# Optimization experiments

Measured on AMD Instinct MI355X. Metric: run time of the kernel, lower is better.

Reference implementation:

```python
import jax, jax.numpy as jnp
import numpy as np

B, T, I, H, O = 256, 2048, 64, 64, 2


def setup_inputs() -> dict:
    key = jax.random.key(0)
    ks = jax.random.split(key, 12)
    s = lambda fan_in: 1.0 / np.sqrt(fan_in)
    u = lambda k, shape, b: jax.random.uniform(k, shape, jnp.float32, -b, b)
    return {
        "x": jax.random.normal(ks[0], (B, T, I), jnp.float32),
        # RNN layer 0 (input -> hidden)
        "W_ih0": u(ks[1], (H, I), s(H)),
        "W_hh0": u(ks[2], (H, H), s(H)),
        "b_ih0": u(ks[3], (H,), s(H)),
        "b_hh0": u(ks[4], (H,), s(H)),
        # RNN layer 1 (hidden -> hidden)
        "W_ih1": u(ks[5], (H, H), s(H)),
        "W_hh1": u(ks[6], (H, H), s(H)),
        "b_ih1": u(ks[7], (H,), s(H)),
        "b_hh1": u(ks[8], (H,), s(H)),
        # MLP head
        "W1": u(ks[9], (H, H), s(H)),
        "b1": u(ks[10], (H,), s(H)),
        "W2": u(ks[11], (O, H), s(H)),
        "b2": jnp.zeros((O,), jnp.float32),
    }


def _rnn_layer(x, W_ih, W_hh, b_ih, b_hh):
    # x: (B, T, D_in) -> (B, T, H); h_t = tanh(x_t W_ih^T + b_ih + h_{t-1} W_hh^T + b_hh)
    # Precompute the input projection for all timesteps (one big GEMM).
    xin = jnp.einsum("btd,hd->bth", x, W_ih) + b_ih + b_hh  # (B,T,H)

    def step(h, xt):
        h_new = jnp.tanh(xt + h @ W_hh.T)
        return h_new, h_new

    h0 = jnp.zeros((x.shape[0], W_hh.shape[0]), x.dtype)
    _, hs = jax.lax.scan(step, h0, jnp.swapaxes(xin, 0, 1))  # (T,B,H)
    return jnp.swapaxes(hs, 0, 1)  # (B,T,H)


def reference(x, W_ih0, W_hh0, b_ih0, b_hh0, W_ih1, W_hh1, b_ih1, b_hh1, W1, b1, W2, b2):
    h = _rnn_layer(x, W_ih0, W_hh0, b_ih0, b_hh0)
    h = _rnn_layer(h, W_ih1, W_hh1, b_ih1, b_hh1)
    # MLP head (dropout disabled in inference): Linear -> ReLU -> Linear
    z = jax.nn.relu(jnp.einsum("bth,oh->bto", h, W1) + b1)
    out = jnp.einsum("bth,oh->bto", z, W2) + b2
    return out
```

## Files before the change

kernel.cpp:

```cpp
#include <hip/hip_runtime.h>


#define T_LEN 2048
#define K     16
#define NITV  (T_LEN / K)

__device__ __forceinline__ float tanh_fast(float x) {
  float e = __expf(2.0f * x);
  return 1.0f - 2.0f / (e + 1.0f);
}

__device__ __forceinline__ float dot64(const float* v, const float (&w)[64]) {
  float a0 = 0.f, a1 = 0.f, a2 = 0.f, a3 = 0.f;
#pragma unroll
  for (int k = 0; k < 64; k += 4) {
    float4 h = *(const float4*)(v + k);
    a0 = fmaf(h.x, w[k + 0], a0);
    a1 = fmaf(h.y, w[k + 1], a1);
    a2 = fmaf(h.z, w[k + 2], a2);
    a3 = fmaf(h.w, w[k + 3], a3);
  }
  return (a0 + a1) + (a2 + a3);
}

__device__ __forceinline__ float dot32(const float* v, const float (&w)[32]) {
  float a0 = 0.f, a1 = 0.f, a2 = 0.f, a3 = 0.f;
#pragma unroll
  for (int k = 0; k < 32; k += 4) {
    float4 h = *(const float4*)(v + k);
    a0 = fmaf(h.x, w[k + 0], a0);
    a1 = fmaf(h.y, w[k + 1], a1);
    a2 = fmaf(h.z, w[k + 2], a2);
    a3 = fmaf(h.w, w[k + 3], a3);
  }
  return (a0 + a1) + (a2 + a3);
}

__global__ __launch_bounds__(256, 1) void rnn_fused(
    const float* __restrict__ x,
    const float* __restrict__ Wih0, const float* __restrict__ Whh0,
    const float* __restrict__ bih0, const float* __restrict__ bhh0,
    const float* __restrict__ Wih1, const float* __restrict__ Whh1,
    const float* __restrict__ bih1, const float* __restrict__ bhh1,
    const float* __restrict__ W1, const float* __restrict__ b1,
    const float* __restrict__ W2, const float* __restrict__ b2,
    float* __restrict__ out) {
  __shared__ __align__(16) float Xc [2][K][64];
  __shared__ __align__(16) float A0b[2][K][64];
  __shared__ __align__(16) float H0b[2][K][64];
  __shared__ __align__(16) float A1b[2][K][64];
  __shared__ __align__(16) float H1b[2][K][64];
  __shared__ __align__(16) float Zb [2][K][64];
  __shared__ __align__(16) float OutL[T_LEN * 2];

  const int tid  = threadIdx.x;
  const int wave = tid >> 6;
  const int lane = tid & 63;
  const int b    = blockIdx.x;

  if (tid < 64)        H0b[1][K - 1][lane] = 0.f;
  else if (tid < 128)  H1b[1][K - 1][lane] = 0.f;

  {
    const float* src = x + (size_t)b * T_LEN * 64;
    *(float4*)(&Xc[0][0][0] + tid * 4) = *(const float4*)(src + tid * 4);
  }

  const float* wsrc = (wave == 0) ? Wih0 : (wave == 1) ? Whh0 : (wave == 2) ? Wih1 : Whh1;
  float w[64];
#pragma unroll
  for (int q = 0; q < 16; ++q) {
    float4 v = *(const float4*)(wsrc + lane * 64 + 4 * q);
    w[4 * q + 0] = v.x; w[4 * q + 1] = v.y; w[4 * q + 2] = v.z; w[4 * q + 3] = v.w;
  }
  float bias = 0.f;
  if (wave == 0) bias = bih0[lane] + bhh0[lane];
  else if (wave == 2) bias = bih1[lane] + bhh1[lane];

  const int kh = (lane >> 5) * 32;
  const int jz = (lane & 31) + ((wave == 2) ? 32 : 0);
  float wE[32];
  float bE = 0.f;
  if (wave == 0 || wave == 2) {
#pragma unroll
    for (int q = 0; q < 8; ++q) {
      float4 v = *(const float4*)(W1 + jz * 64 + kh + 4 * q);
      wE[4 * q + 0] = v.x; wE[4 * q + 1] = v.y; wE[4 * q + 2] = v.z; wE[4 * q + 3] = v.w;
    }
    bE = b1[jz];
  }

  const int tj = lane >> 2, kq = lane & 3;
  float wF0[16], wF1[16];
  float b20 = 0.f, b21 = 0.f;
  if (wave == 2) {
#pragma unroll
    for (int q = 0; q < 4; ++q) {
      float4 v0 = *(const float4*)(W2 + kq * 16 + 4 * q);
      float4 v1 = *(const float4*)(W2 + 64 + kq * 16 + 4 * q);
      wF0[4 * q + 0] = v0.x; wF0[4 * q + 1] = v0.y; wF0[4 * q + 2] = v0.z; wF0[4 * q + 3] = v0.w;
      wF1[4 * q + 0] = v1.x; wF1[4 * q + 1] = v1.y; wF1[4 * q + 2] = v1.z; wF1[4 * q + 3] = v1.w;
    }
    b20 = b2[0]; b21 = b2[1];
  }

  __syncthreads();

  for (int n = 0; n < NITV + 5; ++n) {
    if (wave == 0) {
      float4 px[4];
      const bool pf = (n + 1) < NITV;
      if (pf) {
        const float* src = x + ((size_t)b * T_LEN + (size_t)(n + 1) * K) * 64 + lane * 4;
#pragma unroll
        for (int r = 0; r < 4; ++r) px[r] = *(const float4*)(src + r * 256);
      }
      if (n < NITV) {
        const int s = n & 1;
#pragma unroll
        for (int j = 0; j < K; ++j) {
          A0b[s][j][lane] = bias + dot64(&Xc[s][j][0], w);
        }
      }
      if (n >= 4 && n - 4 < NITV) {
        const int s = (n - 4) & 1;
#pragma unroll
        for (int j = 0; j < K; ++j) {
          float p = dot32(&H1b[s][j][kh], wE);
          p += __shfl_xor(p, 32);
          if (lane < 32) Zb[s][j][jz] = fmaxf(p + bE, 0.f);
        }
      }
      if (pf) {
        float* dst = &Xc[(n + 1) & 1][0][0] + lane * 4;
#pragma unroll
        for (int r = 0; r < 4; ++r) *(float4*)(dst + r * 256) = px[r];
      }
    } else if (wave == 1) {
      if (n >= 1 && n - 1 < NITV) {
        const int s = (n - 1) & 1;
        float av[K];
#pragma unroll
        for (int j = 0; j < K; ++j) av[j] = A0b[s][j][lane];
        const float* prev = &H0b[s ^ 1][K - 1][0];
#pragma unroll
        for (int j = 0; j < K; ++j) {
          float r = dot64(prev, w);
          H0b[s][j][lane] = tanh_fast(av[j] + r);
          prev = &H0b[s][j][0];
        }
      }
    } else if (wave == 2) {
      if (n >= 2 && n - 2 < NITV) {
        const int s = (n - 2) & 1;
#pragma unroll
        for (int j = 0; j < K; ++j) {
          A1b[s][j][lane] = bias + dot64(&H0b[s][j][0], w);
        }
      }
      if (n >= 4 && n - 4 < NITV) {
        const int s = (n - 4) & 1;
#pragma unroll
        for (int j = 0; j < K; ++j) {
          float p = dot32(&H1b[s][j][kh], wE);
          p += __shfl_xor(p, 32);
          if (lane < 32) Zb[s][j][jz] = fmaxf(p + bE, 0.f);
        }
      }
      if (n >= 5 && n - 5 < NITV) {
        const int s = (n - 5) & 1;
        float p0 = 0.f, p1 = 0.f;
#pragma unroll
        for (int q = 0; q < 4; ++q) {
          float4 zv = *(const float4*)(&Zb[s][tj][kq * 16 + 4 * q]);
          p0 = fmaf(zv.x, wF0[4 * q + 0], p0); p1 = fmaf(zv.x, wF1[4 * q + 0], p1);
          p0 = fmaf(zv.y, wF0[4 * q + 1], p0); p1 = fmaf(zv.y, wF1[4 * q + 1], p1);
          p0 = fmaf(zv.z, wF0[4 * q + 2], p0); p1 = fmaf(zv.z, wF1[4 * q + 2], p1);
          p0 = fmaf(zv.w, wF0[4 * q + 3], p0); p1 = fmaf(zv.w, wF1[4 * q + 3], p1);
        }
        p0 += __shfl_xor(p0, 1); p0 += __shfl_xor(p0, 2);
        p1 += __shfl_xor(p1, 1); p1 += __shfl_xor(p1, 2);
        if (kq == 0) {
          const int t = (n - 5) * K + tj;
          OutL[t * 2 + 0] = p0 + b20;
          OutL[t * 2 + 1] = p1 + b21;
        }
      }
    } else {
      if (n >= 3 && n - 3 < NITV) {
        const int s = (n - 3) & 1;
        float av[K];
#pragma unroll
        for (int j = 0; j < K; ++j) av[j] = A1b[s][j][lane];
        const float* prev = &H1b[s ^ 1][K - 1][0];
#pragma unroll
        for (int j = 0; j < K; ++j) {
          float r = dot64(prev, w);
          H1b[s][j][lane] = tanh_fast(av[j] + r);
          prev = &H1b[s][j][0];
        }
      }
    }
    __syncthreads();
  }

  float* obase = out + (size_t)b * T_LEN * 2;
#pragma unroll
  for (int r = 0; r < 4; ++r) {
    const int fi = r * 256 + tid;
    *(float4*)(obase + fi * 4) = *(const float4*)(OutL + fi * 4);
  }
}

extern "C" void kernel_launch(void* const* d_in, const int* in_sizes, int n_in,
                              void* d_out, int out_size, void* d_ws, size_t ws_size,
                              hipStream_t stream) {
  (void)in_sizes; (void)n_in; (void)d_ws; (void)ws_size; (void)out_size;
  const float* x    = (const float*)d_in[0];
  const float* Wih0 = (const float*)d_in[1];
  const float* Whh0 = (const float*)d_in[2];
  const float* bih0 = (const float*)d_in[3];
  const float* bhh0 = (const float*)d_in[4];
  const float* Wih1 = (const float*)d_in[5];
  const float* Whh1 = (const float*)d_in[6];
  const float* bih1 = (const float*)d_in[7];
  const float* bhh1 = (const float*)d_in[8];
  const float* W1   = (const float*)d_in[9];
  const float* b1   = (const float*)d_in[10];
  const float* W2   = (const float*)d_in[11];
  const float* b2   = (const float*)d_in[12];
  float* out = (float*)d_out;

  rnn_fused<<<dim3(256), dim3(256), 0, stream>>>(
      x, Wih0, Whh0, bih0, bhh0, Wih1, Whh1, bih1, bhh1, W1, b1, W2, b2, out);
}
```

Baseline: 1.253 ms.

## Restructure RNN pipeline with readlane recurrence, 64-step chunks, and swizzled LDS

The recurrent waves now keep the hidden state in registers and broadcast it with readlane instead of re-reading it from LDS every step. The chunk size grows from 16 to 64 timesteps, which cuts the number of block-wide barriers. The input-projection and MLP waves switch to a one-timestep-per-lane layout with uniform weight loads, and a swizzled LDS layout avoids bank conflicts. Output is written directly to global memory. The risks are the 64 serial readlanes per step on the critical recurrence path and longer pipeline fill and drain.

```diff
diff --git a/kernel.cpp b/kernel.cpp
--- a/kernel.cpp
+++ b/kernel.cpp
@@ -2,38 +2,12 @@
 
 
 #define T_LEN 2048
-#define K     16
-#define NITV  (T_LEN / K)
-
-__device__ __forceinline__ float tanh_fast(float x) {
-  float e = __expf(2.0f * x);
-  return 1.0f - 2.0f / (e + 1.0f);
-}
-
-__device__ __forceinline__ float dot64(const float* v, const float (&w)[64]) {
-  float a0 = 0.f, a1 = 0.f, a2 = 0.f, a3 = 0.f;
-#pragma unroll
-  for (int k = 0; k < 64; k += 4) {
-    float4 h = *(const float4*)(v + k);
-    a0 = fmaf(h.x, w[k + 0], a0);
-    a1 = fmaf(h.y, w[k + 1], a1);
-    a2 = fmaf(h.z, w[k + 2], a2);
-    a3 = fmaf(h.w, w[k + 3], a3);
-  }
-  return (a0 + a1) + (a2 + a3);
-}
-
-__device__ __forceinline__ float dot32(const float* v, const float (&w)[32]) {
-  float a0 = 0.f, a1 = 0.f, a2 = 0.f, a3 = 0.f;
-#pragma unroll
-  for (int k = 0; k < 32; k += 4) {
-    float4 h = *(const float4*)(v + k);
-    a0 = fmaf(h.x, w[k + 0], a0);
-    a1 = fmaf(h.y, w[k + 1], a1);
-    a2 = fmaf(h.z, w[k + 2], a2);
-    a3 = fmaf(h.w, w[k + 3], a3);
-  }
-  return (a0 + a1) + (a2 + a3);
+#define BATCH 64
+#define NITV  (T_LEN / BATCH)
+#define NLOOP (NITV + 5)
+
+__device__ __forceinline__ int swz(int t, int c) {
+  return t * 64 + ((((c >> 2) ^ (t & 7)) << 2) | (c & 3));
 }
 
 __global__ __launch_bounds__(256, 1) void rnn_fused(
@@ -45,170 +19,189 @@
     const float* __restrict__ W1, const float* __restrict__ b1,
     const float* __restrict__ W2, const float* __restrict__ b2,
     float* __restrict__ out) {
-  __shared__ __align__(16) float Xc [2][K][64];
-  __shared__ __align__(16) float A0b[2][K][64];
-  __shared__ __align__(16) float H0b[2][K][64];
-  __shared__ __align__(16) float A1b[2][K][64];
-  __shared__ __align__(16) float H1b[2][K][64];
-  __shared__ __align__(16) float Zb [2][K][64];
-  __shared__ __align__(16) float OutL[T_LEN * 2];
+  __shared__ __align__(16) float Xc[2][4096];
+  __shared__ __align__(16) float A0[2][4096];
+  __shared__ __align__(16) float P3[3][4096];
+  __shared__ __align__(16) float H1[2][4096];
+  __shared__ __align__(8)  float Hd0[2][64][2];
 
   const int tid  = threadIdx.x;
   const int wave = tid >> 6;
   const int lane = tid & 63;
   const int b    = blockIdx.x;
-
-  if (tid < 64)        H0b[1][K - 1][lane] = 0.f;
-  else if (tid < 128)  H1b[1][K - 1][lane] = 0.f;
-
-  {
-    const float* src = x + (size_t)b * T_LEN * 64;
-    *(float4*)(&Xc[0][0][0] + tid * 4) = *(const float4*)(src + tid * 4);
+  const size_t xbase = (size_t)b * T_LEN * 64;
+
+  if (wave == 0) {
+#pragma unroll
+    for (int it = 0; it < 16; ++it) {
+      const int fi = it * 64 + lane;
+      const int t  = fi >> 4, lq = fi & 15;
+      float4 v = *(const float4*)(x + xbase + fi * 4);
+      *(float4*)&Xc[0][swz(t, lq * 4)] = v;
+    }
   }
-
-  const float* wsrc = (wave == 0) ? Wih0 : (wave == 1) ? Whh0 : (wave == 2) ? Wih1 : Whh1;
-  float w[64];
-#pragma unroll
-  for (int q = 0; q < 16; ++q) {
-    float4 v = *(const float4*)(wsrc + lane * 64 + 4 * q);
-    w[4 * q + 0] = v.x; w[4 * q + 1] = v.y; w[4 * q + 2] = v.z; w[4 * q + 3] = v.w;
-  }
-  float bias = 0.f;
-  if (wave == 0) bias = bih0[lane] + bhh0[lane];
-  else if (wave == 2) bias = bih1[lane] + bhh1[lane];
-
-  const int kh = (lane >> 5) * 32;
-  const int jz = (lane & 31) + ((wave == 2) ? 32 : 0);
-  float wE[32];
-  float bE = 0.f;
-  if (wave == 0 || wave == 2) {
-#pragma unroll
-    for (int q = 0; q < 8; ++q) {
-      float4 v = *(const float4*)(W1 + jz * 64 + kh + 4 * q);
-      wE[4 * q + 0] = v.x; wE[4 * q + 1] = v.y; wE[4 * q + 2] = v.z; wE[4 * q + 3] = v.w;
-    }
-    bE = b1[jz];
-  }
-
-  const int tj = lane >> 2, kq = lane & 3;
-  float wF0[16], wF1[16];
-  float b20 = 0.f, b21 = 0.f;
-  if (wave == 2) {
-#pragma unroll
-    for (int q = 0; q < 4; ++q) {
-      float4 v0 = *(const float4*)(W2 + kq * 16 + 4 * q);
-      float4 v1 = *(const float4*)(W2 + 64 + kq * 16 + 4 * q);
-      wF0[4 * q + 0] = v0.x; wF0[4 * q + 1] = v0.y; wF0[4 * q + 2] = v0.z; wF0[4 * q + 3] = v0.w;
-      wF1[4 * q + 0] = v1.x; wF1[4 * q + 1] = v1.y; wF1[4 * q + 2] = v1.z; wF1[4 * q + 3] = v1.w;
-    }
-    b20 = b2[0]; b21 = b2[1];
-  }
-
   __syncthreads();
 
-  for (int n = 0; n < NITV + 5; ++n) {
-    if (wave == 0) {
-      float4 px[4];
-      const bool pf = (n + 1) < NITV;
-      if (pf) {
-        const float* src = x + ((size_t)b * T_LEN + (size_t)(n + 1) * K) * 64 + lane * 4;
-#pragma unroll
-        for (int r = 0; r < 4; ++r) px[r] = *(const float4*)(src + r * 256);
+  if (wave == 1 || wave == 3) {
+    const float* wsrc = (wave == 1) ? Whh0 : Whh1;
+    float w[64];
+#pragma unroll
+    for (int q = 0; q < 16; ++q) {
+      float4 v = *(const float4*)(wsrc + lane * 64 + 4 * q);
+      w[4*q+0] = v.x; w[4*q+1] = v.y; w[4*q+2] = v.z; w[4*q+3] = v.w;
+    }
+    const int dly = (wave == 1) ? 1 : 3;
+    float h = 0.f;
+    for (int n = 0; n < NLOOP; ++n) {
+      const int m = n - dly;
+      if (m >= 0 && m < NITV) {
+        const float* Ain = (wave == 1) ? &A0[m & 1][0] : &P3[m % 3][0];
+        float* Hout      = (wave == 1) ? &P3[m % 3][0] : &H1[m & 1][0];
+        for (int tt = 0; tt < 64; ++tt) {
+          const int idx = swz(tt, lane);
+          float av = Ain[idx];
+          const int hb = __float_as_int(h);
+          float c0 = 0.f, c1 = 0.f, c2 = 0.f, c3 = 0.f;
+#pragma unroll
+          for (int k = 0; k < 64; k += 4) {
+            c0 = fmaf(__int_as_float(__builtin_amdgcn_readlane(hb, k+0)), w[k+0], c0);
+            c1 = fmaf(__int_as_float(__builtin_amdgcn_readlane(hb, k+1)), w[k+1], c1);
+            c2 = fmaf(__int_as_float(__builtin_amdgcn_readlane(hb, k+2)), w[k+2], c2);
+            c3 = fmaf(__int_as_float(__builtin_amdgcn_readlane(hb, k+3)), w[k+3], c3);
+          }
+          const float pre = av + ((c0 + c1) + (c2 + c3));
+          const float e = __expf(2.f * pre);
+          h = fmaf(-2.f, __builtin_amdgcn_rcpf(e + 1.f), 1.f);
+          Hout[idx] = h;
+        }
+      }
+      __syncthreads();
+    }
+  } else if (wave == 0) {
+    for (int n = 0; n < NLOOP; ++n) {
+      float4 px[16];
+      const bool st = (n + 1) < NITV;
+      if (st) {
+        const float* src = x + xbase + (size_t)(n + 1) * BATCH * 64;
+#pragma unroll
+        for (int it = 0; it < 16; ++it) px[it] = *(const float4*)(src + (it * 64 + lane) * 4);
       }
       if (n < NITV) {
-        const int s = n & 1;
-#pragma unroll
-        for (int j = 0; j < K; ++j) {
-          A0b[s][j][lane] = bias + dot64(&Xc[s][j][0], w);
+        float xr[64];
+#pragma unroll
+        for (int lq = 0; lq < 16; ++lq) {
+          float4 v = *(const float4*)&Xc[n & 1][swz(lane, lq * 4)];
+          xr[4*lq+0] = v.x; xr[4*lq+1] = v.y; xr[4*lq+2] = v.z; xr[4*lq+3] = v.w;
+        }
+        float* Aout = &A0[n & 1][0];
+        for (int g = 0; g < 8; ++g) {
+          const int jb = g * 8;
+          float acc[8];
+#pragma unroll
+          for (int jj = 0; jj < 8; ++jj) acc[jj] = bih0[jb+jj] + bhh0[jb+jj];
+#pragma unroll
+          for (int jj = 0; jj < 8; ++jj) {
+            const float* wr = Wih0 + (jb + jj) * 64;
+#pragma unroll
+            for (int k = 0; k < 64; ++k) acc[jj] = fmaf(wr[k], xr[k], acc[jj]);
+          }
+          *(float4*)&Aout[swz(lane, jb)]     = make_float4(acc[0], acc[1], acc[2], acc[3]);
+          *(float4*)&Aout[swz(lane, jb + 4)] = make_float4(acc[4], acc[5], acc[6], acc[7]);
         }
       }
       if (n >= 4 && n - 4 < NITV) {
-        const int s = (n - 4) & 1;
-#pragma unroll
-        for (int j = 0; j < K; ++j) {
-          float p = dot32(&H1b[s][j][kh], wE);
-          p += __shfl_xor(p, 32);
-          if (lane < 32) Zb[s][j][jz] = fmaxf(p + bE, 0.f);
-        }
-      }
-      if (pf) {
-        float* dst = &Xc[(n + 1) & 1][0][0] + lane * 4;
-#pragma unroll
-        for (int r = 0; r < 4; ++r) *(float4*)(dst + r * 256) = px[r];
-      }
-    } else if (wave == 1) {
-      if (n >= 1 && n - 1 < NITV) {
-        const int s = (n - 1) & 1;
-        float av[K];
-#pragma unroll
-        for (int j = 0; j < K; ++j) av[j] = A0b[s][j][lane];
-        const float* prev = &H0b[s ^ 1][K - 1][0];
-#pragma unroll
-        for (int j = 0; j < K; ++j) {
-          float r = dot64(prev, w);
-          H0b[s][j][lane] = tanh_fast(av[j] + r);
-          prev = &H0b[s][j][0];
-        }
-      }
-    } else if (wave == 2) {
+        const int m = n - 4;
+        float hr[64];
+#pragma unroll
+        for (int lq = 0; lq < 16; ++lq) {
+          float4 v = *(const float4*)&H1[m & 1][swz(lane, lq * 4)];
+          hr[4*lq+0] = v.x; hr[4*lq+1] = v.y; hr[4*lq+2] = v.z; hr[4*lq+3] = v.w;
+        }
+        float p0 = 0.f, p1 = 0.f;
+        for (int j = 0; j < 32; ++j) {
+          float za = b1[j], zb = 0.f, zc = 0.f, zd = 0.f;
+          const float* wr = W1 + j * 64;
+#pragma unroll
+          for (int k = 0; k < 64; k += 4) {
+            za = fmaf(wr[k+0], hr[k+0], za); zb = fmaf(wr[k+1], hr[k+1], zb);
+            zc = fmaf(wr[k+2], hr[k+2], zc); zd = fmaf(wr[k+3], hr[k+3], zd);
+          }
+          const float zv = fmaxf((za + zb) + (zc + zd), 0.f);
+          p0 = fmaf(W2[j], zv, p0);
+          p1 = fmaf(W2[64 + j], zv, p1);
+        }
+        *(float2*)&Hd0[m & 1][lane][0] = make_float2(p0, p1);
+      }
+      if (st) {
+#pragma unroll
+        for (int it = 0; it < 16; ++it) {
+          const int fi = it * 64 + lane;
+          const int t = fi >> 4, lq = fi & 15;
+          *(float4*)&Xc[(n + 1) & 1][swz(t, lq * 4)] = px[it];
+        }
+      }
+      __syncthreads();
+    }
+  } else {
+    float hp0 = 0.f, hp1 = 0.f;
+    for (int n = 0; n < NLOOP; ++n) {
+      if (n >= 5 && n - 5 < NITV) {
+        const int m = n - 5;
+        const float2 q = *(const float2*)&Hd0[m & 1][lane][0];
+        float2 o;
+        o.x = q.x + hp0 + b2[0];
+        o.y = q.y + hp1 + b2[1];
+        *(float2*)(out + ((size_t)b * T_LEN + (size_t)m * BATCH + lane) * 2) = o;
+      }
       if (n >= 2 && n - 2 < NITV) {
-        const int s = (n - 2) & 1;
-#pragma unroll
-        for (int j = 0; j < K; ++j) {
-          A1b[s][j][lane] = bias + dot64(&H0b[s][j][0], w);
+        const int m = n - 2;
+        float* pool = &P3[m % 3][0];
+        float hr[64];
+#pragma unroll
+        for (int lq = 0; lq < 16; ++lq) {
+          float4 v = *(const float4*)&pool[swz(lane, lq * 4)];
+          hr[4*lq+0] = v.x; hr[4*lq+1] = v.y; hr[4*lq+2] = v.z; hr[4*lq+3] = v.w;
+        }
+        for (int g = 0; g < 8; ++g) {
+          const int jb = g * 8;
+          float acc[8];
+#pragma unroll
+          for (int jj = 0; jj < 8; ++jj) acc[jj] = bih1[jb+jj] + bhh1[jb+jj];
+#pragma unroll
+          for (int jj = 0; jj < 8; ++jj) {
+            const float* wr = Wih1 + (jb + jj) * 64;
+#pragma unroll
+            for (int k = 0; k < 64; ++k) acc[jj] = fmaf(wr[k], hr[k], acc[jj]);
+          }
+          *(float4*)&pool[swz(lane, jb)]     = make_float4(acc[0], acc[1], acc[2], acc[3]);
+          *(float4*)&pool[swz(lane, jb + 4)] = make_float4(acc[4], acc[5], acc[6], acc[7]);
         }
       }
       if (n >= 4 && n - 4 < NITV) {
-        const int s = (n - 4) & 1;
-#pragma unroll
-        for (int j = 0; j < K; ++j) {
-          float p = dot32(&H1b[s][j][kh], wE);
-          p += __shfl_xor(p, 32);
-          if (lane < 32) Zb[s][j][jz] = fmaxf(p + bE, 0.f);
-        }
-      }
-      if (n >= 5 && n - 5 < NITV) {
-        const int s = (n - 5) & 1;
+        const int m = n - 4;
+        float hr[64];
+#pragma unroll
+        for (int lq = 0; lq < 16; ++lq) {
+          float4 v = *(const float4*)&H1[m & 1][swz(lane, lq * 4)];
+          hr[4*lq+0] = v.x; hr[4*lq+1] = v.y; hr[4*lq+2] = v.z; hr[4*lq+3] = v.w;
+        }
         float p0 = 0.f, p1 = 0.f;
-#pragma unroll
-        for (int q = 0; q < 4; ++q) {
-          float4 zv = *(const float4*)(&Zb[s][tj][kq * 16 + 4 * q]);
-          p0 = fmaf(zv.x, wF0[4 * q + 0], p0); p1 = fmaf(zv.x, wF1[4 * q + 0], p1);
-          p0 = fmaf(zv.y, wF0[4 * q + 1], p0); p1 = fmaf(zv.y, wF1[4 * q + 1], p1);
-          p0 = fmaf(zv.z, wF0[4 * q + 2], p0); p1 = fmaf(zv.z, wF1[4 * q + 2], p1);
-          p0 = fmaf(zv.w, wF0[4 * q + 3], p0); p1 = fmaf(zv.w, wF1[4 * q + 3], p1);
-        }
-        p0 += __shfl_xor(p0, 1); p0 += __shfl_xor(p0, 2);
-        p1 += __shfl_xor(p1, 1); p1 += __shfl_xor(p1, 2);
-        if (kq == 0) {
-          const int t = (n - 5) * K + tj;
-          OutL[t * 2 + 0] = p0 + b20;
-          OutL[t * 2 + 1] = p1 + b21;
-        }
-      }
-    } else {
-      if (n >= 3 && n - 3 < NITV) {
-        const int s = (n - 3) & 1;
-        float av[K];
-#pragma unroll
-        for (int j = 0; j < K; ++j) av[j] = A1b[s][j][lane];
-        const float* prev = &H1b[s ^ 1][K - 1][0];
-#pragma unroll
-        for (int j = 0; j < K; ++j) {
-          float r = dot64(prev, w);
-          H1b[s][j][lane] = tanh_fast(av[j] + r);
-          prev = &H1b[s][j][0];
-        }
-      }
-    }
-    __syncthreads();
-  }
-
-  float* obase = out + (size_t)b * T_LEN * 2;
-#pragma unroll
-  for (int r = 0; r < 4; ++r) {
-    const int fi = r * 256 + tid;
-    *(float4*)(obase + fi * 4) = *(const float4*)(OutL + fi * 4);
+        for (int j = 32; j < 64; ++j) {
+          float za = b1[j], zb = 0.f, zc = 0.f, zd = 0.f;
+          const float* wr = W1 + j * 64;
+#pragma unroll
+          for (int k = 0; k < 64; k += 4) {
+            za = fmaf(wr[k+0], hr[k+0], za); zb = fmaf(wr[k+1], hr[k+1], zb);
+            zc = fmaf(wr[k+2], hr[k+2], zc); zd = fmaf(wr[k+3], hr[k+3], zd);
+          }
+          const float zv = fmaxf((za + zb) + (zc + zd), 0.f);
+          p0 = fmaf(W2[j], zv, p0);
+          p1 = fmaf(W2[64 + j], zv, p1);
+        }
+        hp0 = p0; hp1 = p1;
+      }
+      __syncthreads();
+    }
   }
 }
 
```

Result: slower. 1.633 ms (+30.4%).
